# Optimization experiments

Hardware: AMD Instinct MI355X
Metric: run time of the kernel (lower is better)

## Reference

```python
import jax, jax.numpy as jnp
import numpy as np

D = 512; H = 2048; NH = 8; NL = 6; VX = 32000; VY = 32000
B = 256; SX = 15; SY = 17; PAD = 0; DH = D // NH


def _pe_table(seq_len, d):
    pos = np.arange(seq_len, dtype=np.float32)[:, None]
    div = 1.0 / (10000.0 ** (np.arange(0, d, 2, dtype=np.float32) / d))
    pe = np.zeros((seq_len, d), dtype=np.float32)
    pe[:, 0::2] = np.sin(pos * div)
    pe[:, 1::2] = np.cos(pos * div)
    return jnp.asarray(pe)


def _ln(x, g, b, eps=1e-5):
    m = x.mean(-1, keepdims=True)
    v = ((x - m) ** 2).mean(-1, keepdims=True)
    return g * (x - m) / jnp.sqrt(v + eps) + b


def _attn(xq, xkv, mask, w, b):
    # w: [4, D, D] (q,k,v,o), b: [4, D]; mask broadcastable to [B,NH,Sq,Sk]
    bs, sq, _ = xq.shape
    sk = xkv.shape[1]
    q = (xq @ w[0] + b[0]).reshape(bs, sq, NH, DH).transpose(0, 2, 1, 3)
    k = (xkv @ w[1] + b[1]).reshape(bs, sk, NH, DH).transpose(0, 2, 1, 3)
    v = (xkv @ w[2] + b[2]).reshape(bs, sk, NH, DH).transpose(0, 2, 1, 3)
    s = jnp.einsum('bhqd,bhkd->bhqk', q, k) / np.sqrt(float(DH))
    s = jnp.where(mask == 0.0, -1e9, s)
    p = jax.nn.softmax(s, axis=-1)
    o = jnp.einsum('bhqk,bhkd->bhqd', p, v).transpose(0, 2, 1, 3).reshape(bs, sq, D)
    return o @ w[3] + b[3]


def setup_inputs():
    key = jax.random.key(0)
    ks = jax.random.split(key, 24)
    s = 0.02
    x = jax.random.randint(ks[0], (B, SX), 0, VX)
    y = jax.random.randint(ks[1], (B, SY), 0, VY)
    emb_x = (jax.random.normal(ks[2], (VX, D)) * s).at[PAD].set(0.0)
    emb_y = (jax.random.normal(ks[3], (VY, D)) * s).at[PAD].set(0.0)
    inp = dict(x=x, y=y, emb_x=emb_x, emb_y=emb_y)
    inp['enc_attn_w'] = jax.random.normal(ks[4], (NL, 4, D, D)) * s
    inp['enc_attn_b'] = jnp.zeros((NL, 4, D))
    inp['enc_ln'] = jnp.stack([jnp.ones((NL, 2, D)), jnp.zeros((NL, 2, D))], axis=2)  # [NL,2,2,D] (g,b)
    inp['enc_ffn_w0'] = jax.random.normal(ks[5], (NL, D, H)) * s
    inp['enc_ffn_b0'] = jnp.zeros((NL, H))
    inp['enc_ffn_w1'] = jax.random.normal(ks[6], (NL, H, D)) * s
    inp['enc_ffn_b1'] = jnp.zeros((NL, D))
    inp['dec_attn_w'] = jax.random.normal(ks[7], (NL, 8, D, D)) * s  # self q,k,v,o then cross q,k,v,o
    inp['dec_attn_b'] = jnp.zeros((NL, 8, D))
    inp['dec_ln'] = jnp.stack([jnp.ones((NL, 3, D)), jnp.zeros((NL, 3, D))], axis=2)  # [NL,3,2,D]
    inp['dec_ffn_w0'] = jax.random.normal(ks[8], (NL, D, H)) * s
    inp['dec_ffn_b0'] = jnp.zeros((NL, H))
    inp['dec_ffn_w1'] = jax.random.normal(ks[9], (NL, H, D)) * s
    inp['dec_ffn_b1'] = jnp.zeros((NL, D))
    inp['fc_w'] = jax.random.normal(ks[10], (D, VY)) * s
    inp['fc_b'] = jnp.zeros((VY,))
    return inp


def reference(x, y, emb_x, emb_y, enc_attn_w, enc_attn_b, enc_ln,
              enc_ffn_w0, enc_ffn_b0, enc_ffn_w1, enc_ffn_b1,
              dec_attn_w, dec_attn_b, dec_ln,
              dec_ffn_w0, dec_ffn_b0, dec_ffn_w1, dec_ffn_b1,
              fc_w, fc_b):
    pe = _pe_table(max(SX, SY + 1), D)
    mask_x = (x != PAD).astype(jnp.float32)[:, None, None, :]        # [B,1,1,SX]
    mask_pad = (y != PAD).astype(jnp.float32)[:, None, None, :]       # [B,1,1,SY]
    mask_y = mask_pad * jnp.tril(jnp.ones((SY, SY), jnp.float32))     # [B,1,SY,SY]

    hx = emb_x[x] + pe[:SX]
    for i in range(NL):
        a = _attn(hx, hx, mask_x, enc_attn_w[i], enc_attn_b[i])
        h0 = _ln(hx + a, enc_ln[i, 0, 0], enc_ln[i, 0, 1])
        f = jax.nn.relu(h0 @ enc_ffn_w0[i] + enc_ffn_b0[i]) @ enc_ffn_w1[i] + enc_ffn_b1[i]
        hx = _ln(h0 + f, enc_ln[i, 1, 0], enc_ln[i, 1, 1])

    hy = emb_y[y] + pe[:SY]
    for i in range(NL):
        a = _attn(hy, hy, mask_y, dec_attn_w[i, :4], dec_attn_b[i, :4])
        h0 = _ln(hy + a, dec_ln[i, 0, 0], dec_ln[i, 0, 1])
        c = _attn(h0, hx, mask_x, dec_attn_w[i, 4:], dec_attn_b[i, 4:])
        h1 = _ln(h0 + c, dec_ln[i, 1, 0], dec_ln[i, 1, 1])
        f = jax.nn.relu(h1 @ dec_ffn_w0[i] + dec_ffn_b0[i]) @ dec_ffn_w1[i] + dec_ffn_b1[i]
        hy = _ln(h1 + f, dec_ln[i, 2, 0], dec_ln[i, 2, 1])

    return hy @ fc_w + fc_b  # [B, SY, VY]
```

## Files before the change

### kernel.cpp

```cpp
#include <hip/hip_runtime.h>
#include <hip/hip_bf16.h>
#include <stdint.h>
#include <type_traits>

typedef __hip_bfloat16 bf16;
typedef __attribute__((ext_vector_type(8))) short bf16x8;
typedef __attribute__((ext_vector_type(4))) float f32x4;

#define DMODEL 512
#define HFF    2048
#define NHEADS 8
#define NLAYERS 6
#define DHEAD  64
#define BATCH  256
#define SXLEN  15
#define SYLEN  17

__device__ __forceinline__ float us2f(unsigned short u) {
  union { unsigned int i; float f; } c; c.i = ((unsigned int)u) << 16; return c.f;
}
__device__ __forceinline__ unsigned short f2us(float f) {
  bf16 h = __float2bfloat16(f);
  return *reinterpret_cast<unsigned short*>(&h);
}
__device__ __forceinline__ float b2f(bf16 v) { return __bfloat162float(v); }

__device__ __forceinline__ void gload_lds16(const void* g, void* l) {
  __builtin_amdgcn_global_load_lds(
      (const __attribute__((address_space(1))) unsigned int*)g,
      (__attribute__((address_space(3))) unsigned int*)l, 16, 0, 0);
}

template<int RELU, int MT, int NT, int WM, int WN, int ZMAP, typename OT>
__global__ __launch_bounds__(WM * WN * 64) void gemm_t(
    const bf16* __restrict__ A, const bf16* __restrict__ Wt,
    const float* __restrict__ bias, OT* __restrict__ C,
    int M, int N, int K,
    long long wStride, long long bStride, long long cStride)
{
  constexpr int BK  = 64;
  constexpr int TH  = WM * WN * 64;
  constexpr int RB  = BK * 2;
  constexpr int MF  = MT / WM / 16;
  constexpr int NF  = NT / WN / 16;
  constexpr int WRS = MT / WM;
  constexpr int WCS = NT / WN;
  constexpr int ABY = MT * RB;
  constexpr int BBY = NT * RB;

  const int z = blockIdx.z;
  if (ZMAP == 1) {
    int idx = (z >> 1) * 8 + 5 + (z & 1);
    Wt   += (long long)idx * wStride;
    bias += (long long)idx * bStride;
  } else {
    Wt   += (long long)z * wStride;
    bias += (long long)z * bStride;
  }
  C += (long long)z * cStride;

  __shared__ __align__(16) char lds[ABY + BBY];
  const int t    = threadIdx.x;
  const int m0   = blockIdx.y * MT, n0 = blockIdx.x * NT;
  const int wid  = t >> 6, lane = t & 63;
  const int wm   = wid / WN, wn = wid % WN;
  const int g    = lane >> 4, r = lane & 15;

  f32x4 acc[MF][NF];
  #pragma unroll
  for (int i = 0; i < MF; ++i)
    #pragma unroll
    for (int j = 0; j < NF; ++j) acc[i][j] = (f32x4)0.f;

  const char* Ab = (const char*)(A  + (long long)m0 * K);
  const char* Bb = (const char*)(Wt + (long long)n0 * K);
  const int rowBytes = K * 2;

  for (int kt = 0; kt < K; kt += BK) {
    __syncthreads();
    #pragma unroll
    for (int off = 0; off < ABY; off += TH * 16) {
      int o = off + t * 16;
      gload_lds16(Ab + (long long)(o / RB) * rowBytes + kt * 2 + (o % RB), lds + o);
    }
    #pragma unroll
    for (int off = 0; off < BBY; off += TH * 16) {
      int o = off + t * 16;
      gload_lds16(Bb + (long long)(o / RB) * rowBytes + kt * 2 + (o % RB), lds + ABY + o);
    }
    __syncthreads();

    #pragma unroll
    for (int kh = 0; kh < BK / 32; ++kh) {
      bf16x8 af[MF], bfr[NF];
      #pragma unroll
      for (int ms = 0; ms < MF; ++ms)
        af[ms] = *(const bf16x8*)(lds + (wm * WRS + ms * 16 + r) * RB + kh * 64 + g * 16);
      #pragma unroll
      for (int ns = 0; ns < NF; ++ns)
        bfr[ns] = *(const bf16x8*)(lds + ABY + (wn * WCS + ns * 16 + r) * RB + kh * 64 + g * 16);
      #pragma unroll
      for (int ms = 0; ms < MF; ++ms)
        #pragma unroll
        for (int ns = 0; ns < NF; ++ns)
          acc[ms][ns] = __builtin_amdgcn_mfma_f32_16x16x32_bf16(af[ms], bfr[ns], acc[ms][ns], 0, 0, 0);
    }
  }

  #pragma unroll
  for (int ms = 0; ms < MF; ++ms) {
    int rowb = m0 + wm * WRS + ms * 16 + g * 4;
    #pragma unroll
    for (int ns = 0; ns < NF; ++ns) {
      int col = n0 + wn * WCS + ns * 16 + r;
      float bv = bias[col];
      f32x4 v = acc[ms][ns];
      #pragma unroll
      for (int j = 0; j < 4; ++j) {
        float o = v[j] + bv;
        if (RELU) o = fmaxf(o, 0.f);
        if constexpr (std::is_same<OT, float>::value)
          C[(long long)(rowb + j) * N + col] = o;
        else
          C[(long long)(rowb + j) * N + col] = __float2bfloat16(o);
      }
    }
  }
}

__global__ __launch_bounds__(256) void transpose_cast(
    const float* __restrict__ in, bf16* __restrict__ out, int K, int N)
{
  __shared__ unsigned short tile[32][33];
  long long base = (long long)blockIdx.z * K * N;
  const float* ip = in + base;
  unsigned short* op = (unsigned short*)out + base;
  int nx = blockIdx.x * 32, ky = blockIdx.y * 32;
  int tx = threadIdx.x, ty = threadIdx.y;
  #pragma unroll
  for (int j = 0; j < 4; ++j)
    tile[ty + j * 8][tx] = f2us(ip[(long long)(ky + ty + j * 8) * N + nx + tx]);
  __syncthreads();
  #pragma unroll
  for (int j = 0; j < 4; ++j)
    op[(long long)(nx + ty + j * 8) * K + ky + tx] = tile[tx][ty + j * 8];
}

__global__ __launch_bounds__(64) void embed2_k(
    const int* __restrict__ xids, const int* __restrict__ yids,
    const float* __restrict__ ex, const float* __restrict__ ey,
    bf16* __restrict__ ox, bf16* __restrict__ oy)
{
  int row = blockIdx.x;
  const int* ids; const float* emb; bf16* out; int S;
  if (row < BATCH * SXLEN) { ids = xids; emb = ex; out = ox; S = SXLEN; }
  else { row -= BATCH * SXLEN; ids = yids; emb = ey; out = oy; S = SYLEN; }
  int s = row % S;
  int lane = threadIdx.x;
  int id = ids[row];
  const float* e = emb + (long long)id * DMODEL;
  unsigned short* o = (unsigned short*)(out + (long long)row * DMODEL);
  #pragma unroll
  for (int j = 0; j < 8; ++j) {
    int d  = lane * 8 + j;
    int jj = d >> 1;
    float freq = __expf(-(float)(2 * jj) * (9.210340371976184f / 512.f));
    float ang  = (float)s * freq;
    float pe   = (d & 1) ? cosf(ang) : sinf(ang);
    o[d] = f2us(e[d] + pe);
  }
}

template<int CAUSAL>
__global__ __launch_bounds__(64) void attn_core(
    const bf16* __restrict__ Q, const bf16* __restrict__ Kk, const bf16* __restrict__ V,
    const int* __restrict__ tok, bf16* __restrict__ O, int Sq, int Sk)
{
  int bh = blockIdx.x; int b = bh >> 3; int h = bh & 7;
  __shared__ float Qs[SYLEN][DHEAD + 1], Ks[SYLEN][DHEAD + 1], Vs[SYLEN][DHEAD + 1];
  __shared__ float P[SYLEN][SYLEN + 1];
  __shared__ float msk[SYLEN];
  int t = threadIdx.x;

  for (int idx = t; idx < Sq * DHEAD; idx += 64) {
    int q = idx >> 6, d = idx & 63;
    Qs[q][d] = b2f(Q[((long long)(b * Sq + q)) * DMODEL + h * DHEAD + d]);
  }
  for (int idx = t; idx < Sk * DHEAD; idx += 64) {
    int k = idx >> 6, d = idx & 63;
    Ks[k][d] = b2f(Kk[((long long)(b * Sk + k)) * DMODEL + h * DHEAD + d]);
    Vs[k][d] = b2f(V [((long long)(b * Sk + k)) * DMODEL + h * DHEAD + d]);
  }
  if (t < Sk) msk[t] = (tok[b * Sk + t] != 0) ? 1.f : 0.f;
  __syncthreads();

  for (int idx = t; idx < Sq * Sk; idx += 64) {
    int q = idx / Sk, k = idx - q * Sk;
    float s = 0.f;
    #pragma unroll
    for (int i = 0; i < DHEAD; ++i) s += Qs[q][i] * Ks[k][i];
    s *= 0.125f;
    bool m = (msk[k] != 0.f) && (!CAUSAL || k <= q);
    P[q][k] = m ? s : -1e9f;
  }
  __syncthreads();

  if (t < Sq) {
    float mx = -1e30f;
    for (int k = 0; k < Sk; ++k) mx = fmaxf(mx, P[t][k]);
    float sum = 0.f;
    for (int k = 0; k < Sk; ++k) { float e = __expf(P[t][k] - mx); P[t][k] = e; sum += e; }
    float inv = 1.f / sum;
    for (int k = 0; k < Sk; ++k) P[t][k] *= inv;
  }
  __syncthreads();

  int d = t;
  for (int q = 0; q < Sq; ++q) {
    float o = 0.f;
    for (int k = 0; k < Sk; ++k) o += P[q][k] * Vs[k][d];
    O[((long long)(b * Sq + q)) * DMODEL + h * DHEAD + d] = __float2bfloat16(o);
  }
}

__global__ __launch_bounds__(64) void add_ln_k(
    const bf16* __restrict__ a, const bf16* __restrict__ b,
    const float* __restrict__ gam, const float* __restrict__ bet,
    bf16* __restrict__ out)
{
  long long row = blockIdx.x;
  int lane = threadIdx.x;
  union { uint4 u; unsigned short s[8]; } ua, ub, uo;
  ua.u = ((const uint4*)(a + row * DMODEL))[lane];
  ub.u = ((const uint4*)(b + row * DMODEL))[lane];
  float x[8]; float s = 0.f, sq = 0.f;
  #pragma unroll
  for (int j = 0; j < 8; ++j) {
    x[j] = us2f(ua.s[j]) + us2f(ub.s[j]);
    s += x[j]; sq += x[j] * x[j];
  }
  #pragma unroll
  for (int o = 32; o > 0; o >>= 1) { s += __shfl_xor(s, o); sq += __shfl_xor(sq, o); }
  float mean = s * (1.f / DMODEL);
  float var  = sq * (1.f / DMODEL) - mean * mean;
  float inv  = rsqrtf(var + 1e-5f);
  float4 g0 = ((const float4*)gam)[lane * 2], g1 = ((const float4*)gam)[lane * 2 + 1];
  float4 b0 = ((const float4*)bet)[lane * 2], b1 = ((const float4*)bet)[lane * 2 + 1];
  float gg[8] = {g0.x, g0.y, g0.z, g0.w, g1.x, g1.y, g1.z, g1.w};
  float bb[8] = {b0.x, b0.y, b0.z, b0.w, b1.x, b1.y, b1.z, b1.w};
  #pragma unroll
  for (int j = 0; j < 8; ++j)
    uo.s[j] = f2us(gg[j] * (x[j] - mean) * inv + bb[j]);
  ((uint4*)(out + row * DMODEL))[lane] = uo.u;
}

extern "C" void kernel_launch(void* const* d_in, const int* in_sizes, int n_in,
                              void* d_out, int out_size, void* d_ws, size_t ws_size,
                              hipStream_t stream)
{
  const int*   x        = (const int*)  d_in[0];
  const int*   y        = (const int*)  d_in[1];
  const float* emb_x    = (const float*)d_in[2];
  const float* emb_y    = (const float*)d_in[3];
  const float* enc_attn_w = (const float*)d_in[4];
  const float* enc_attn_b = (const float*)d_in[5];
  const float* enc_ln     = (const float*)d_in[6];
  const float* enc_f0w    = (const float*)d_in[7];
  const float* enc_f0b    = (const float*)d_in[8];
  const float* enc_f1w    = (const float*)d_in[9];
  const float* enc_f1b    = (const float*)d_in[10];
  const float* dec_attn_w = (const float*)d_in[11];
  const float* dec_attn_b = (const float*)d_in[12];
  const float* dec_ln     = (const float*)d_in[13];
  const float* dec_f0w    = (const float*)d_in[14];
  const float* dec_f0b    = (const float*)d_in[15];
  const float* dec_f1w    = (const float*)d_in[16];
  const float* dec_f1b    = (const float*)d_in[17];
  const float* fc_w       = (const float*)d_in[18];
  const float* fc_b       = (const float*)d_in[19];

  const int MX = BATCH * SXLEN;
  const int MY = BATCH * SYLEN;
  const long long DD = (long long)DMODEL * DMODEL;
  const long long SMEL = (long long)MY * DMODEL;
  const long long MXEL = (long long)MX * DMODEL;

  char* p = (char*)d_ws;
  auto alloc = [&](long long elems) -> bf16* {
    bf16* r = (bf16*)p; p += ((elems * 2 + 255) / 256) * 256; return r;
  };
  bf16* wt_enc_attn = alloc(24 * DD);
  bf16* wt_dec_attn = alloc(48 * DD);
  bf16* wt_enc_f0   = alloc(6LL * DMODEL * HFF);
  bf16* wt_enc_f1   = alloc(6LL * DMODEL * HFF);
  bf16* wt_dec_f0   = alloc(6LL * DMODEL * HFF);
  bf16* wt_dec_f1   = alloc(6LL * DMODEL * HFF);
  bf16* wt_fc       = alloc(32000LL * DMODEL);
  bf16* hx  = alloc(SMEL);
  bf16* hy  = alloc(SMEL);
  bf16* qb  = alloc(3 * SMEL);
  bf16* ao  = alloc(SMEL);
  bf16* h0  = alloc(SMEL);
  bf16* h1  = alloc(SMEL);
  bf16* mid = alloc((long long)MY * HFF);
  bf16* ckv = alloc(12 * MXEL);
  if ((size_t)(p - (char*)d_ws) > ws_size) return;

  dim3 tb(32, 8);
  transpose_cast<<<dim3(16, 16, 24), tb, 0, stream>>>(enc_attn_w, wt_enc_attn, DMODEL, DMODEL);
  transpose_cast<<<dim3(16, 16, 48), tb, 0, stream>>>(dec_attn_w, wt_dec_attn, DMODEL, DMODEL);
  transpose_cast<<<dim3(64, 16, 6),  tb, 0, stream>>>(enc_f0w, wt_enc_f0, DMODEL, HFF);
  transpose_cast<<<dim3(16, 64, 6),  tb, 0, stream>>>(enc_f1w, wt_enc_f1, HFF, DMODEL);
  transpose_cast<<<dim3(64, 16, 6),  tb, 0, stream>>>(dec_f0w, wt_dec_f0, DMODEL, HFF);
  transpose_cast<<<dim3(16, 64, 6),  tb, 0, stream>>>(dec_f1w, wt_dec_f1, HFF, DMODEL);
  transpose_cast<<<dim3(1000, 16, 1), tb, 0, stream>>>(fc_w, wt_fc, DMODEL, 32000);

  embed2_k<<<MX + MY, 64, 0, stream>>>(x, y, emb_x, emb_y, hx, hy);

  for (int i = 0; i < NLAYERS; ++i) {
    const bf16*  Wl = wt_enc_attn + (long long)i * 4 * DD;
    const float* Bl = enc_attn_b + (long long)i * 4 * DMODEL;
    const float* Lg = enc_ln + (size_t)i * 2048;
    gemm_t<0, 64, 64, 2, 1, 0, bf16><<<dim3(8, 60, 3), 128, 0, stream>>>(hx, Wl, Bl, qb,
        MX, DMODEL, DMODEL, DD, DMODEL, SMEL);
    attn_core<0><<<BATCH * NHEADS, 64, 0, stream>>>(qb, qb + SMEL, qb + 2 * SMEL, x, ao, SXLEN, SXLEN);
    gemm_t<0, 64, 64, 2, 1, 0, bf16><<<dim3(8, 60, 1), 128, 0, stream>>>(ao, Wl + 3 * DD, Bl + 3 * DMODEL, h1,
        MX, DMODEL, DMODEL, 0, 0, 0);
    add_ln_k<<<MX, 64, 0, stream>>>(hx, h1, Lg, Lg + 512, h0);
    gemm_t<1, 64, 64, 2, 1, 0, bf16><<<dim3(32, 60, 1), 128, 0, stream>>>(h0, wt_enc_f0 + (long long)i * DMODEL * HFF,
        enc_f0b + (long long)i * HFF, mid, MX, HFF, DMODEL, 0, 0, 0);
    gemm_t<0, 64, 64, 2, 1, 0, bf16><<<dim3(8, 60, 1), 128, 0, stream>>>(mid, wt_enc_f1 + (long long)i * DMODEL * HFF,
        enc_f1b + (long long)i * DMODEL, h1, MX, DMODEL, HFF, 0, 0, 0);
    add_ln_k<<<MX, 64, 0, stream>>>(h0, h1, Lg + 1024, Lg + 1536, hx);
  }

  gemm_t<0, 64, 64, 2, 1, 1, bf16><<<dim3(8, 60, 12), 128, 0, stream>>>(hx, wt_dec_attn,
      dec_attn_b, ckv, MX, DMODEL, DMODEL, DD, DMODEL, MXEL);

  for (int i = 0; i < NLAYERS; ++i) {
    const bf16*  Wl = wt_dec_attn + (long long)i * 8 * DD;
    const float* Bl = dec_attn_b + (long long)i * 8 * DMODEL;
    const float* Lg = dec_ln + (size_t)i * 3072;
    gemm_t<0, 64, 64, 2, 1, 0, bf16><<<dim3(8, 68, 3), 128, 0, stream>>>(hy, Wl, Bl, qb,
        MY, DMODEL, DMODEL, DD, DMODEL, SMEL);
    attn_core<1><<<BATCH * NHEADS, 64, 0, stream>>>(qb, qb + SMEL, qb + 2 * SMEL, y, ao, SYLEN, SYLEN);
    gemm_t<0, 64, 64, 2, 1, 0, bf16><<<dim3(8, 68, 1), 128, 0, stream>>>(ao, Wl + 3 * DD, Bl + 3 * DMODEL, h1,
        MY, DMODEL, DMODEL, 0, 0, 0);
    add_ln_k<<<MY, 64, 0, stream>>>(hy, h1, Lg, Lg + 512, h0);
    gemm_t<0, 64, 64, 2, 1, 0, bf16><<<dim3(8, 68, 1), 128, 0, stream>>>(h0, Wl + 4 * DD, Bl + 4 * DMODEL, qb,
        MY, DMODEL, DMODEL, 0, 0, 0);
    attn_core<0><<<BATCH * NHEADS, 64, 0, stream>>>(qb, ckv + (long long)(2 * i) * MXEL,
        ckv + (long long)(2 * i + 1) * MXEL, x, ao, SYLEN, SXLEN);
    gemm_t<0, 64, 64, 2, 1, 0, bf16><<<dim3(8, 68, 1), 128, 0, stream>>>(ao, Wl + 7 * DD, Bl + 7 * DMODEL, h1,
        MY, DMODEL, DMODEL, 0, 0, 0);
    add_ln_k<<<MY, 64, 0, stream>>>(h0, h1, Lg + 1024, Lg + 1536, h0);
    gemm_t<1, 64, 64, 2, 1, 0, bf16><<<dim3(32, 68, 1), 128, 0, stream>>>(h0, wt_dec_f0 + (long long)i * DMODEL * HFF,
        dec_f0b + (long long)i * HFF, mid, MY, HFF, DMODEL, 0, 0, 0);
    gemm_t<0, 64, 64, 2, 1, 0, bf16><<<dim3(8, 68, 1), 128, 0, stream>>>(mid, wt_dec_f1 + (long long)i * DMODEL * HFF,
        dec_f1b + (long long)i * DMODEL, h1, MY, DMODEL, HFF, 0, 0, 0);
    add_ln_k<<<MY, 64, 0, stream>>>(h0, h1, Lg + 2048, Lg + 2560, hy);
  }

  gemm_t<0, 128, 128, 2, 2, 0, float><<<dim3(250, 34, 1), 256, 0, stream>>>(hy, wt_fc, fc_b,
      (float*)d_out, MY, 32000, DMODEL, 0, 0, 0);
}
```

Measured before the change: 2.084 ms.

## Fuse output-projection and FFN-down GEMMs with residual add and LayerNorm

```diff
diff --git a/kernel.cpp b/kernel.cpp
--- a/kernel.cpp
+++ b/kernel.cpp
@@ -128,6 +128,109 @@
   }
 }
 
+__global__ __launch_bounds__(256) void gemm_ln(
+    const bf16* __restrict__ A, const bf16* __restrict__ Wt,
+    const float* __restrict__ bias, const bf16* __restrict__ R,
+    const float* __restrict__ gam, const float* __restrict__ bet,
+    bf16* __restrict__ Out, int K)
+{
+  __shared__ __align__(16) char lds[34304];
+  const int t   = threadIdx.x;
+  const int m0  = blockIdx.x * 16;
+  const int wid = t >> 6, lane = t & 63;
+  const int g   = lane >> 4, r = lane & 15;
+
+  f32x4 acc[8];
+  #pragma unroll
+  for (int ns = 0; ns < 8; ++ns) acc[ns] = (f32x4)0.f;
+
+  const char* Ab = (const char*)A + (long long)m0 * K * 2;
+  const char* Bb = (const char*)Wt;
+  const int rowBytes = K * 2;
+
+  for (int kt = 0; kt < K; kt += 32) {
+    __syncthreads();
+    if (t < 64)
+      gload_lds16(Ab + (long long)(t >> 2) * rowBytes + kt * 2 + (t & 3) * 16, lds + t * 16);
+    #pragma unroll
+    for (int off = 0; off < 32768; off += 4096) {
+      int o = off + t * 16;
+      gload_lds16(Bb + (long long)(o >> 6) * rowBytes + kt * 2 + (o & 63), lds + 1024 + o);
+    }
+    __syncthreads();
+    bf16x8 af = *(const bf16x8*)(lds + r * 64 + g * 16);
+    #pragma unroll
+    for (int ns = 0; ns < 8; ++ns) {
+      int n = wid * 128 + ns * 16 + r;
+      bf16x8 bfv = *(const bf16x8*)(lds + 1024 + n * 64 + g * 16);
+      acc[ns] = __builtin_amdgcn_mfma_f32_16x16x32_bf16(af, bfv, acc[ns], 0, 0, 0);
+    }
+  }
+  __syncthreads();
+  {
+    const char* Rb = (const char*)R + (long long)m0 * 1024;
+    #pragma unroll
+    for (int off = 0; off < 16384; off += 4096) {
+      int o = off + t * 16;
+      gload_lds16(Rb + o, lds + 1024 + o);
+    }
+  }
+  __syncthreads();
+
+  const unsigned short* Rl = (const unsigned short*)(lds + 1024);
+  float* red = (float*)(lds + 17408);
+  float s[4] = {0.f, 0.f, 0.f, 0.f}, sq[4] = {0.f, 0.f, 0.f, 0.f};
+  #pragma unroll
+  for (int ns = 0; ns < 8; ++ns) {
+    int col = wid * 128 + ns * 16 + r;
+    float bv = bias[col];
+    #pragma unroll
+    for (int j = 0; j < 4; ++j) {
+      int rr = g * 4 + j;
+      float v = acc[ns][j] + bv + us2f(Rl[rr * 512 + col]);
+      acc[ns][j] = v;
+      s[j] += v; sq[j] += v * v;
+    }
+  }
+  #pragma unroll
+  for (int m = 1; m <= 8; m <<= 1) {
+    #pragma unroll
+    for (int j = 0; j < 4; ++j) { s[j] += __shfl_xor(s[j], m); sq[j] += __shfl_xor(sq[j], m); }
+  }
+  if (r == 0) {
+    #pragma unroll
+    for (int j = 0; j < 4; ++j) {
+      red[((wid * 4 + g) * 4 + j) * 2 + 0] = s[j];
+      red[((wid * 4 + g) * 4 + j) * 2 + 1] = sq[j];
+    }
+  }
+  __syncthreads();
+  float mean[4], inv[4];
+  #pragma unroll
+  for (int j = 0; j < 4; ++j) {
+    float ts = 0.f, tq = 0.f;
+    #pragma unroll
+    for (int w = 0; w < 4; ++w) {
+      ts += red[((w * 4 + g) * 4 + j) * 2 + 0];
+      tq += red[((w * 4 + g) * 4 + j) * 2 + 1];
+    }
+    mean[j] = ts * (1.f / 512.f);
+    float var = tq * (1.f / 512.f) - mean[j] * mean[j];
+    inv[j] = rsqrtf(var + 1e-5f);
+  }
+  unsigned short* Ob = (unsigned short*)Out + (long long)m0 * 512;
+  #pragma unroll
+  for (int ns = 0; ns < 8; ++ns) {
+    int col = wid * 128 + ns * 16 + r;
+    float gv = gam[col], bv = bet[col];
+    #pragma unroll
+    for (int j = 0; j < 4; ++j) {
+      int rr = g * 4 + j;
+      Ob[(long long)rr * 512 + col] = f2us(gv * (acc[ns][j] - mean[j]) * inv[j] + bv);
+    }
+  }
+}
+
 __global__ __launch_bounds__(256) void transpose_cast(
     const float* __restrict__ in, bf16* __restrict__ out, int K, int N)
 {
@@ -221,37 +324,6 @@
     for (int k = 0; k < Sk; ++k) o += P[q][k] * Vs[k][d];
     O[((long long)(b * Sq + q)) * DMODEL + h * DHEAD + d] = __float2bfloat16(o);
   }
-}
-
-__global__ __launch_bounds__(64) void add_ln_k(
-    const bf16* __restrict__ a, const bf16* __restrict__ b,
-    const float* __restrict__ gam, const float* __restrict__ bet,
-    bf16* __restrict__ out)
-{
-  long long row = blockIdx.x;
-  int lane = threadIdx.x;
-  union { uint4 u; unsigned short s[8]; } ua, ub, uo;
-  ua.u = ((const uint4*)(a + row * DMODEL))[lane];
-  ub.u = ((const uint4*)(b + row * DMODEL))[lane];
-  float x[8]; float s = 0.f, sq = 0.f;
-  #pragma unroll
-  for (int j = 0; j < 8; ++j) {
-    x[j] = us2f(ua.s[j]) + us2f(ub.s[j]);
-    s += x[j]; sq += x[j] * x[j];
-  }
-  #pragma unroll
-  for (int o = 32; o > 0; o >>= 1) { s += __shfl_xor(s, o); sq += __shfl_xor(sq, o); }
-  float mean = s * (1.f / DMODEL);
-  float var  = sq * (1.f / DMODEL) - mean * mean;
-  float inv  = rsqrtf(var + 1e-5f);
-  float4 g0 = ((const float4*)gam)[lane * 2], g1 = ((const float4*)gam)[lane * 2 + 1];
-  float4 b0 = ((const float4*)bet)[lane * 2], b1 = ((const float4*)bet)[lane * 2 + 1];
-  float gg[8] = {g0.x, g0.y, g0.z, g0.w, g1.x, g1.y, g1.z, g1.w};
-  float bb[8] = {b0.x, b0.y, b0.z, b0.w, b1.x, b1.y, b1.z, b1.w};
-  #pragma unroll
-  for (int j = 0; j < 8; ++j)
-    uo.s[j] = f2us(gg[j] * (x[j] - mean) * inv + bb[j]);
-  ((uint4*)(out + row * DMODEL))[lane] = uo.u;
 }
 
 extern "C" void kernel_launch(void* const* d_in, const int* in_sizes, int n_in,
@@ -324,14 +396,12 @@
     gemm_t<0, 64, 64, 2, 1, 0, bf16><<<dim3(8, 60, 3), 128, 0, stream>>>(hx, Wl, Bl, qb,
         MX, DMODEL, DMODEL, DD, DMODEL, SMEL);
     attn_core<0><<<BATCH * NHEADS, 64, 0, stream>>>(qb, qb + SMEL, qb + 2 * SMEL, x, ao, SXLEN, SXLEN);
-    gemm_t<0, 64, 64, 2, 1, 0, bf16><<<dim3(8, 60, 1), 128, 0, stream>>>(ao, Wl + 3 * DD, Bl + 3 * DMODEL, h1,
-        MX, DMODEL, DMODEL, 0, 0, 0);
-    add_ln_k<<<MX, 64, 0, stream>>>(hx, h1, Lg, Lg + 512, h0);
+    gemm_ln<<<MX / 16, 256, 0, stream>>>(ao, Wl + 3 * DD, Bl + 3 * DMODEL, hx,
+        Lg, Lg + 512, h0, DMODEL);
     gemm_t<1, 64, 64, 2, 1, 0, bf16><<<dim3(32, 60, 1), 128, 0, stream>>>(h0, wt_enc_f0 + (long long)i * DMODEL * HFF,
         enc_f0b + (long long)i * HFF, mid, MX, HFF, DMODEL, 0, 0, 0);
-    gemm_t<0, 64, 64, 2, 1, 0, bf16><<<dim3(8, 60, 1), 128, 0, stream>>>(mid, wt_enc_f1 + (long long)i * DMODEL * HFF,
-        enc_f1b + (long long)i * DMODEL, h1, MX, DMODEL, HFF, 0, 0, 0);
-    add_ln_k<<<MX, 64, 0, stream>>>(h0, h1, Lg + 1024, Lg + 1536, hx);
+    gemm_ln<<<MX / 16, 256, 0, stream>>>(mid, wt_enc_f1 + (long long)i * DMODEL * HFF,
+        enc_f1b + (long long)i * DMODEL, h0, Lg + 1024, Lg + 1536, hx, HFF);
   }
 
   gemm_t<0, 64, 64, 2, 1, 1, bf16><<<dim3(8, 60, 12), 128, 0, stream>>>(hx, wt_dec_attn,
@@ -344,21 +414,18 @@
     gemm_t<0, 64, 64, 2, 1, 0, bf16><<<dim3(8, 68, 3), 128, 0, stream>>>(hy, Wl, Bl, qb,
         MY, DMODEL, DMODEL, DD, DMODEL, SMEL);
     attn_core<1><<<BATCH * NHEADS, 64, 0, stream>>>(qb, qb + SMEL, qb + 2 * SMEL, y, ao, SYLEN, SYLEN);
-    gemm_t<0, 64, 64, 2, 1, 0, bf16><<<dim3(8, 68, 1), 128, 0, stream>>>(ao, Wl + 3 * DD, Bl + 3 * DMODEL, h1,
-        MY, DMODEL, DMODEL, 0, 0, 0);
-    add_ln_k<<<MY, 64, 0, stream>>>(hy, h1, Lg, Lg + 512, h0);
+    gemm_ln<<<MY / 16, 256, 0, stream>>>(ao, Wl + 3 * DD, Bl + 3 * DMODEL, hy,
+        Lg, Lg + 512, h0, DMODEL);
     gemm_t<0, 64, 64, 2, 1, 0, bf16><<<dim3(8, 68, 1), 128, 0, stream>>>(h0, Wl + 4 * DD, Bl + 4 * DMODEL, qb,
         MY, DMODEL, DMODEL, 0, 0, 0);
     attn_core<0><<<BATCH * NHEADS, 64, 0, stream>>>(qb, ckv + (long long)(2 * i) * MXEL,
         ckv + (long long)(2 * i + 1) * MXEL, x, ao, SYLEN, SXLEN);
-    gemm_t<0, 64, 64, 2, 1, 0, bf16><<<dim3(8, 68, 1), 128, 0, stream>>>(ao, Wl + 7 * DD, Bl + 7 * DMODEL, h1,
-        MY, DMODEL, DMODEL, 0, 0, 0);
-    add_ln_k<<<MY, 64, 0, stream>>>(h0, h1, Lg + 1024, Lg + 1536, h0);
-    gemm_t<1, 64, 64, 2, 1, 0, bf16><<<dim3(32, 68, 1), 128, 0, stream>>>(h0, wt_dec_f0 + (long long)i * DMODEL * HFF,
+    gemm_ln<<<MY / 16, 256, 0, stream>>>(ao, Wl + 7 * DD, Bl + 7 * DMODEL, h0,
+        Lg + 1024, Lg + 1536, h1, DMODEL);
+    gemm_t<1, 64, 64, 2, 1, 0, bf16><<<dim3(32, 68, 1), 128, 0, stream>>>(h1, wt_dec_f0 + (long long)i * DMODEL * HFF,
         dec_f0b + (long long)i * HFF, mid, MY, HFF, DMODEL, 0, 0, 0);
-    gemm_t<0, 64, 64, 2, 1, 0, bf16><<<dim3(8, 68, 1), 128, 0, stream>>>(mid, wt_dec_f1 + (long long)i * DMODEL * HFF,
-        dec_f1b + (long long)i * DMODEL, h1, MY, DMODEL, HFF, 0, 0, 0);
-    add_ln_k<<<MY, 64, 0, stream>>>(h0, h1, Lg + 2048, Lg + 2560, hy);
+    gemm_ln<<<MY / 16, 256, 0, stream>>>(mid, wt_dec_f1 + (long long)i * DMODEL * HFF,
+        dec_f1b + (long long)i * DMODEL, h1, Lg + 2048, Lg + 2560, hy, HFF);
   }
 
   gemm_t<0, 128, 128, 2, 2, 0, float><<<dim3(250, 34, 1), 256, 0, stream>>>(hy, wt_fc, fc_b,
```

Result: slower. 2.677 ms (+28.4%).

## Split-K the FFN down-projection with a fused LN reduction, and enlarge FFN-up tiles

Applied to the files above, without the earlier changes.

```diff
diff --git a/kernel.cpp b/kernel.cpp
--- a/kernel.cpp
+++ b/kernel.cpp
@@ -31,11 +31,11 @@
       (__attribute__((address_space(3))) unsigned int*)l, 16, 0, 0);
 }
 
-template<int RELU, int MT, int NT, int WM, int WN, int ZMAP, typename OT>
+template<int RELU, int MT, int NT, int WM, int WN, int ZMAP, int BIAS, typename OT>
 __global__ __launch_bounds__(WM * WN * 64) void gemm_t(
     const bf16* __restrict__ A, const bf16* __restrict__ Wt,
     const float* __restrict__ bias, OT* __restrict__ C,
-    int M, int N, int K,
+    int M, int N, int K, int ldk,
     long long wStride, long long bStride, long long cStride)
 {
   constexpr int BK  = 64;
@@ -49,10 +49,13 @@
   constexpr int BBY = NT * RB;
 
   const int z = blockIdx.z;
+  long long koff = 0;
   if (ZMAP == 1) {
     int idx = (z >> 1) * 8 + 5 + (z & 1);
     Wt   += (long long)idx * wStride;
     bias += (long long)idx * bStride;
+  } else if (ZMAP == 2) {
+    koff = (long long)z * K;
   } else {
     Wt   += (long long)z * wStride;
     bias += (long long)z * bStride;
@@ -72,9 +75,9 @@
     #pragma unroll
     for (int j = 0; j < NF; ++j) acc[i][j] = (f32x4)0.f;
 
-  const char* Ab = (const char*)(A  + (long long)m0 * K);
-  const char* Bb = (const char*)(Wt + (long long)n0 * K);
-  const int rowBytes = K * 2;
+  const char* Ab = (const char*)(A  + (long long)m0 * ldk + koff);
+  const char* Bb = (const char*)(Wt + (long long)n0 * ldk + koff);
+  const int rowBytes = ldk * 2;
 
   for (int kt = 0; kt < K; kt += BK) {
     __syncthreads();
@@ -113,7 +116,7 @@
     #pragma unroll
     for (int ns = 0; ns < NF; ++ns) {
       int col = n0 + wn * WCS + ns * 16 + r;
-      float bv = bias[col];
+      float bv = BIAS ? bias[col] : 0.f;
       f32x4 v = acc[ms][ns];
       #pragma unroll
       for (int j = 0; j < 4; ++j) {
@@ -128,13 +131,15 @@
   }
 }
 
-__global__ __launch_bounds__(256) void transpose_cast(
-    const float* __restrict__ in, bf16* __restrict__ out, int K, int N)
+__global__ __launch_bounds__(256) void transpose_cast2(
+    const float* __restrict__ inA, const float* __restrict__ inB, int zSplit,
+    bf16* __restrict__ out, int K, int N)
 {
   __shared__ unsigned short tile[32][33];
-  long long base = (long long)blockIdx.z * K * N;
-  const float* ip = in + base;
-  unsigned short* op = (unsigned short*)out + base;
+  int z = blockIdx.z;
+  const float* ip = (z < zSplit) ? inA + (long long)z * K * N
+                                 : inB + (long long)(z - zSplit) * K * N;
+  unsigned short* op = (unsigned short*)out + (long long)z * K * N;
   int nx = blockIdx.x * 32, ky = blockIdx.y * 32;
   int tx = threadIdx.x, ty = threadIdx.y;
   #pragma unroll
@@ -237,6 +242,45 @@
   #pragma unroll
   for (int j = 0; j < 8; ++j) {
     x[j] = us2f(ua.s[j]) + us2f(ub.s[j]);
+    s += x[j]; sq += x[j] * x[j];
+  }
+  #pragma unroll
+  for (int o = 32; o > 0; o >>= 1) { s += __shfl_xor(s, o); sq += __shfl_xor(sq, o); }
+  float mean = s * (1.f / DMODEL);
+  float var  = sq * (1.f / DMODEL) - mean * mean;
+  float inv  = rsqrtf(var + 1e-5f);
+  float4 g0 = ((const float4*)gam)[lane * 2], g1 = ((const float4*)gam)[lane * 2 + 1];
+  float4 b0 = ((const float4*)bet)[lane * 2], b1 = ((const float4*)bet)[lane * 2 + 1];
+  float gg[8] = {g0.x, g0.y, g0.z, g0.w, g1.x, g1.y, g1.z, g1.w};
+  float bb[8] = {b0.x, b0.y, b0.z, b0.w, b1.x, b1.y, b1.z, b1.w};
+  #pragma unroll
+  for (int j = 0; j < 8; ++j)
+    uo.s[j] = f2us(gg[j] * (x[j] - mean) * inv + bb[j]);
+  ((uint4*)(out + row * DMODEL))[lane] = uo.u;
+}
+
+__global__ __launch_bounds__(64) void add_ln3_k(
+    const bf16* __restrict__ R, const float* __restrict__ P, long long pStride,
+    const float* __restrict__ bias,
+    const float* __restrict__ gam, const float* __restrict__ bet,
+    bf16* __restrict__ out)
+{
+  long long row = blockIdx.x;
+  int lane = threadIdx.x;
+  union { uint4 u; unsigned short s[8]; } ua, uo;
+  ua.u = ((const uint4*)(R + row * DMODEL))[lane];
+  const float4* p0 = (const float4*)(P + row * DMODEL);
+  const float4* p1 = (const float4*)(P + pStride + row * DMODEL);
+  float4 a0 = p0[lane * 2], a1 = p0[lane * 2 + 1];
+  float4 c0 = p1[lane * 2], c1 = p1[lane * 2 + 1];
+  float4 bi0 = ((const float4*)bias)[lane * 2], bi1 = ((const float4*)bias)[lane * 2 + 1];
+  float pa[8] = {a0.x, a0.y, a0.z, a0.w, a1.x, a1.y, a1.z, a1.w};
+  float pc[8] = {c0.x, c0.y, c0.z, c0.w, c1.x, c1.y, c1.z, c1.w};
+  float pb[8] = {bi0.x, bi0.y, bi0.z, bi0.w, bi1.x, bi1.y, bi1.z, bi1.w};
+  float x[8]; float s = 0.f, sq = 0.f;
+  #pragma unroll
+  for (int j = 0; j < 8; ++j) {
+    x[j] = us2f(ua.s[j]) + pa[j] + pc[j] + pb[j];
     s += x[j]; sq += x[j] * x[j];
   }
   #pragma unroll
@@ -284,18 +328,16 @@
   const long long DD = (long long)DMODEL * DMODEL;
   const long long SMEL = (long long)MY * DMODEL;
   const long long MXEL = (long long)MX * DMODEL;
+  const long long FFEL = (long long)DMODEL * HFF;
 
   char* p = (char*)d_ws;
   auto alloc = [&](long long elems) -> bf16* {
     bf16* r = (bf16*)p; p += ((elems * 2 + 255) / 256) * 256; return r;
   };
-  bf16* wt_enc_attn = alloc(24 * DD);
-  bf16* wt_dec_attn = alloc(48 * DD);
-  bf16* wt_enc_f0   = alloc(6LL * DMODEL * HFF);
-  bf16* wt_enc_f1   = alloc(6LL * DMODEL * HFF);
-  bf16* wt_dec_f0   = alloc(6LL * DMODEL * HFF);
-  bf16* wt_dec_f1   = alloc(6LL * DMODEL * HFF);
-  bf16* wt_fc       = alloc(32000LL * DMODEL);
+  bf16* wt_attn = alloc(72 * DD);
+  bf16* wt_f0   = alloc(12 * FFEL);
+  bf16* wt_f1   = alloc(12 * FFEL);
+  bf16* wt_fc   = alloc(32000LL * DMODEL);
   bf16* hx  = alloc(SMEL);
   bf16* hy  = alloc(SMEL);
   bf16* qb  = alloc(3 * SMEL);
@@ -304,16 +346,21 @@
   bf16* h1  = alloc(SMEL);
   bf16* mid = alloc((long long)MY * HFF);
   bf16* ckv = alloc(12 * MXEL);
+  float* fp = (float*)alloc(2LL * MY * DMODEL * 2);
   if ((size_t)(p - (char*)d_ws) > ws_size) return;
 
+  bf16* wt_enc_attn = wt_attn;
+  bf16* wt_dec_attn = wt_attn + 24 * DD;
+  bf16* wt_enc_f0   = wt_f0;
+  bf16* wt_dec_f0   = wt_f0 + 6 * FFEL;
+  bf16* wt_enc_f1   = wt_f1;
+  bf16* wt_dec_f1   = wt_f1 + 6 * FFEL;
+
   dim3 tb(32, 8);
-  transpose_cast<<<dim3(16, 16, 24), tb, 0, stream>>>(enc_attn_w, wt_enc_attn, DMODEL, DMODEL);
-  transpose_cast<<<dim3(16, 16, 48), tb, 0, stream>>>(dec_attn_w, wt_dec_attn, DMODEL, DMODEL);
-  transpose_cast<<<dim3(64, 16, 6),  tb, 0, stream>>>(enc_f0w, wt_enc_f0, DMODEL, HFF);
-  transpose_cast<<<dim3(16, 64, 6),  tb, 0, stream>>>(enc_f1w, wt_enc_f1, HFF, DMODEL);
-  transpose_cast<<<dim3(64, 16, 6),  tb, 0, stream>>>(dec_f0w, wt_dec_f0, DMODEL, HFF);
-  transpose_cast<<<dim3(16, 64, 6),  tb, 0, stream>>>(dec_f1w, wt_dec_f1, HFF, DMODEL);
-  transpose_cast<<<dim3(1000, 16, 1), tb, 0, stream>>>(fc_w, wt_fc, DMODEL, 32000);
+  transpose_cast2<<<dim3(16, 16, 72), tb, 0, stream>>>(enc_attn_w, dec_attn_w, 24, wt_attn, DMODEL, DMODEL);
+  transpose_cast2<<<dim3(64, 16, 12), tb, 0, stream>>>(enc_f0w, dec_f0w, 6, wt_f0, DMODEL, HFF);
+  transpose_cast2<<<dim3(16, 64, 12), tb, 0, stream>>>(enc_f1w, dec_f1w, 6, wt_f1, HFF, DMODEL);
+  transpose_cast2<<<dim3(1000, 16, 1), tb, 0, stream>>>(fc_w, fc_w, 1, wt_fc, DMODEL, 32000);
 
   embed2_k<<<MX + MY, 64, 0, stream>>>(x, y, emb_x, emb_y, hx, hy);
 
@@ -321,46 +368,48 @@
     const bf16*  Wl = wt_enc_attn + (long long)i * 4 * DD;
     const float* Bl = enc_attn_b + (long long)i * 4 * DMODEL;
     const float* Lg = enc_ln + (size_t)i * 2048;
-    gemm_t<0, 64, 64, 2, 1, 0, bf16><<<dim3(8, 60, 3), 128, 0, stream>>>(hx, Wl, Bl, qb,
-        MX, DMODEL, DMODEL, DD, DMODEL, SMEL);
+    gemm_t<0, 64, 64, 2, 1, 0, 1, bf16><<<dim3(8, 60, 3), 128, 0, stream>>>(hx, Wl, Bl, qb,
+        MX, DMODEL, DMODEL, DMODEL, DD, DMODEL, SMEL);
     attn_core<0><<<BATCH * NHEADS, 64, 0, stream>>>(qb, qb + SMEL, qb + 2 * SMEL, x, ao, SXLEN, SXLEN);
-    gemm_t<0, 64, 64, 2, 1, 0, bf16><<<dim3(8, 60, 1), 128, 0, stream>>>(ao, Wl + 3 * DD, Bl + 3 * DMODEL, h1,
-        MX, DMODEL, DMODEL, 0, 0, 0);
+    gemm_t<0, 64, 64, 2, 1, 0, 1, bf16><<<dim3(8, 60, 1), 128, 0, stream>>>(ao, Wl + 3 * DD, Bl + 3 * DMODEL, h1,
+        MX, DMODEL, DMODEL, DMODEL, 0, 0, 0);
     add_ln_k<<<MX, 64, 0, stream>>>(hx, h1, Lg, Lg + 512, h0);
-    gemm_t<1, 64, 64, 2, 1, 0, bf16><<<dim3(32, 60, 1), 128, 0, stream>>>(h0, wt_enc_f0 + (long long)i * DMODEL * HFF,
-        enc_f0b + (long long)i * HFF, mid, MX, HFF, DMODEL, 0, 0, 0);
-    gemm_t<0, 64, 64, 2, 1, 0, bf16><<<dim3(8, 60, 1), 128, 0, stream>>>(mid, wt_enc_f1 + (long long)i * DMODEL * HFF,
-        enc_f1b + (long long)i * DMODEL, h1, MX, DMODEL, HFF, 0, 0, 0);
-    add_ln_k<<<MX, 64, 0, stream>>>(h0, h1, Lg + 1024, Lg + 1536, hx);
-  }
-
-  gemm_t<0, 64, 64, 2, 1, 1, bf16><<<dim3(8, 60, 12), 128, 0, stream>>>(hx, wt_dec_attn,
-      dec_attn_b, ckv, MX, DMODEL, DMODEL, DD, DMODEL, MXEL);
+    gemm_t<1, 128, 128, 2, 2, 0, 1, bf16><<<dim3(16, 30, 1), 256, 0, stream>>>(h0, wt_enc_f0 + (long long)i * FFEL,
+        enc_f0b + (long long)i * HFF, mid, MX, HFF, DMODEL, DMODEL, 0, 0, 0);
+    gemm_t<0, 64, 64, 2, 1, 2, 0, float><<<dim3(8, 60, 2), 128, 0, stream>>>(mid, wt_enc_f1 + (long long)i * FFEL,
+        enc_f1b, fp, MX, DMODEL, 1024, HFF, 0, 0, (long long)MY * DMODEL);
+    add_ln3_k<<<MX, 64, 0, stream>>>(h0, fp, (long long)MY * DMODEL,
+        enc_f1b + (long long)i * DMODEL, Lg + 1024, Lg + 1536, hx);
+  }
+
+  gemm_t<0, 64, 64, 2, 1, 1, 1, bf16><<<dim3(8, 60, 12), 128, 0, stream>>>(hx, wt_dec_attn,
+      dec_attn_b, ckv, MX, DMODEL, DMODEL, DMODEL, DD, DMODEL, MXEL);
 
   for (int i = 0; i < NLAYERS; ++i) {
     const bf16*  Wl = wt_dec_attn + (long long)i * 8 * DD;
     const float* Bl = dec_attn_b + (long long)i * 8 * DMODEL;
     const float* Lg = dec_ln + (size_t)i * 3072;
-    gemm_t<0, 64, 64, 2, 1, 0, bf16><<<dim3(8, 68, 3), 128, 0, stream>>>(hy, Wl, Bl, qb,
-        MY, DMODEL, DMODEL, DD, DMODEL, SMEL);
+    gemm_t<0, 64, 64, 2, 1, 0, 1, bf16><<<dim3(8, 68, 3), 128, 0, stream>>>(hy, Wl, Bl, qb,
+        MY, DMODEL, DMODEL, DMODEL, DD, DMODEL, SMEL);
     attn_core<1><<<BATCH * NHEADS, 64, 0, stream>>>(qb, qb + SMEL, qb + 2 * SMEL, y, ao, SYLEN, SYLEN);
-    gemm_t<0, 64, 64, 2, 1, 0, bf16><<<dim3(8, 68, 1), 128, 0, stream>>>(ao, Wl + 3 * DD, Bl + 3 * DMODEL, h1,
-        MY, DMODEL, DMODEL, 0, 0, 0);
+    gemm_t<0, 64, 64, 2, 1, 0, 1, bf16><<<dim3(8, 68, 1), 128, 0, stream>>>(ao, Wl + 3 * DD, Bl + 3 * DMODEL, h1,
+        MY, DMODEL, DMODEL, DMODEL, 0, 0, 0);
     add_ln_k<<<MY, 64, 0, stream>>>(hy, h1, Lg, Lg + 512, h0);
-    gemm_t<0, 64, 64, 2, 1, 0, bf16><<<dim3(8, 68, 1), 128, 0, stream>>>(h0, Wl + 4 * DD, Bl + 4 * DMODEL, qb,
-        MY, DMODEL, DMODEL, 0, 0, 0);
+    gemm_t<0, 64, 64, 2, 1, 0, 1, bf16><<<dim3(8, 68, 1), 128, 0, stream>>>(h0, Wl + 4 * DD, Bl + 4 * DMODEL, qb,
+        MY, DMODEL, DMODEL, DMODEL, 0, 0, 0);
     attn_core<0><<<BATCH * NHEADS, 64, 0, stream>>>(qb, ckv + (long long)(2 * i) * MXEL,
         ckv + (long long)(2 * i + 1) * MXEL, x, ao, SYLEN, SXLEN);
-    gemm_t<0, 64, 64, 2, 1, 0, bf16><<<dim3(8, 68, 1), 128, 0, stream>>>(ao, Wl + 7 * DD, Bl + 7 * DMODEL, h1,
-        MY, DMODEL, DMODEL, 0, 0, 0);
+    gemm_t<0, 64, 64, 2, 1, 0, 1, bf16><<<dim3(8, 68, 1), 128, 0, stream>>>(ao, Wl + 7 * DD, Bl + 7 * DMODEL, h1,
+        MY, DMODEL, DMODEL, DMODEL, 0, 0, 0);
     add_ln_k<<<MY, 64, 0, stream>>>(h0, h1, Lg + 1024, Lg + 1536, h0);
-    gemm_t<1, 64, 64, 2, 1, 0, bf16><<<dim3(32, 68, 1), 128, 0, stream>>>(h0, wt_dec_f0 + (long long)i * DMODEL * HFF,
-        dec_f0b + (long long)i * HFF, mid, MY, HFF, DMODEL, 0, 0, 0);
-    gemm_t<0, 64, 64, 2, 1, 0, bf16><<<dim3(8, 68, 1), 128, 0, stream>>>(mid, wt_dec_f1 + (long long)i * DMODEL * HFF,
-        dec_f1b + (long long)i * DMODEL, h1, MY, DMODEL, HFF, 0, 0, 0);
-    add_ln_k<<<MY, 64, 0, stream>>>(h0, h1, Lg + 2048, Lg + 2560, hy);
-  }
-
-  gemm_t<0, 128, 128, 2, 2, 0, float><<<dim3(250, 34, 1), 256, 0, stream>>>(hy, wt_fc, fc_b,
-      (float*)d_out, MY, 32000, DMODEL, 0, 0, 0);
-}
+    gemm_t<1, 128, 128, 2, 2, 0, 1, bf16><<<dim3(16, 34, 1), 256, 0, stream>>>(h0, wt_dec_f0 + (long long)i * FFEL,
+        dec_f0b + (long long)i * HFF, mid, MY, HFF, DMODEL, DMODEL, 0, 0, 0);
+    gemm_t<0, 64, 64, 2, 1, 2, 0, float><<<dim3(8, 68, 2), 128, 0, stream>>>(mid, wt_dec_f1 + (long long)i * FFEL,
+        dec_f1b, fp, MY, DMODEL, 1024, HFF, 0, 0, (long long)MY * DMODEL);
+    add_ln3_k<<<MY, 64, 0, stream>>>(h0, fp, (long long)MY * DMODEL,
+        dec_f1b + (long long)i * DMODEL, Lg + 2048, Lg + 2560, hy);
+  }
+
+  gemm_t<0, 128, 128, 2, 2, 0, 1, float><<<dim3(250, 34, 1), 256, 0, stream>>>(hy, wt_fc, fc_b,
+      (float*)d_out, MY, 32000, DMODEL, DMODEL, 0, 0, 0);
+}
```

After: 2.006 ms. -3.8%, faster.
